# Kernel optimization log

Hardware: AMD Instinct MI355X
Metric: run time of the kernel (lower is better)

The kernel has to match this reference:

```python
import jax, jax.numpy as jnp
import numpy as np

B, T, K = 256, 512, 128


def _reverse_sequence(x, lens, axis_len):
    # Reverse the first lens[b] entries of x[b] along time axis (axis=1); rest unchanged.
    pos = jnp.arange(axis_len)[None, :]              # [1, T]
    idx = jnp.where(pos < lens[:, None], lens[:, None] - 1 - pos, pos)  # [B, T]
    if x.ndim == 3:
        idx = idx[:, :, None]
        idx = jnp.broadcast_to(idx, x.shape)
    return jnp.take_along_axis(x, idx, axis=1)


def setup_inputs() -> dict:
    key = jax.random.key(0)
    k1, k2, k3 = jax.random.split(key, 3)
    potentials = jax.random.normal(k1, (B, T, K), dtype=jnp.float32)
    sequence_lengths = jax.random.randint(k2, (B,), 1, T + 1, dtype=jnp.int32)
    # glorot_uniform for [K, K] transitions
    limit = np.sqrt(6.0 / (K + K))
    transitions = jax.random.uniform(k3, (K, K), dtype=jnp.float32,
                                     minval=-limit, maxval=limit)
    return {"potentials": potentials, "transitions": transitions,
            "sequence_lengths": sequence_lengths}


def _crf_decode(potentials, transitions, sequence_lengths):
    lens = sequence_lengths.astype(jnp.int32)
    num_tags = potentials.shape[-1]
    init_state = potentials[:, 0, :]                 # [B, K]
    inputs = potentials[:, 1:, :]                    # [B, T-1, K]
    lens_m1 = jnp.maximum(0, lens - 1)
    mask = jnp.arange(inputs.shape[1])[None, :] < lens_m1[:, None]  # [B, T-1]

    def fwd_step(state, xm):
        x, m = xm                                    # x [B,K], m [B]
        ts = state[:, :, None] + transitions[None]   # [B, K(prev), K(cur)]
        new_state = x + jnp.max(ts, axis=1)          # [B, K]
        bp = jnp.argmax(ts, axis=1).astype(jnp.int32)
        new_state = jnp.where(m[:, None], new_state, state)
        bp = jnp.where(m[:, None], bp, 0)
        return new_state, bp

    xs = (jnp.swapaxes(inputs, 0, 1), jnp.swapaxes(mask, 0, 1))
    last_score, bps = jax.lax.scan(fwd_step, init_state, xs)
    backpointers = jnp.swapaxes(bps, 0, 1)           # [B, T-1, K]
    backpointers = _reverse_sequence(backpointers, lens_m1, backpointers.shape[1])

    init_tag = jnp.argmax(last_score, axis=1).astype(jnp.int32)  # [B]

    def bwd_step(tag, bp):                           # tag [B], bp [B,K]
        new = jnp.take_along_axis(bp, tag[:, None], axis=1)[:, 0]
        return new, new

    _, tags = jax.lax.scan(bwd_step, init_tag, jnp.swapaxes(backpointers, 0, 1))
    decode_tags = jnp.concatenate([init_tag[:, None], jnp.swapaxes(tags, 0, 1)], axis=1)  # [B,T]
    decode_tags = _reverse_sequence(decode_tags, lens, decode_tags.shape[1])
    best_score = jnp.max(last_score, axis=1)
    return decode_tags, best_score


def reference(potentials, transitions, sequence_lengths):
    decode_tags, _ = _crf_decode(potentials, transitions, sequence_lengths)
    # inference-phase output: one-hot of Viterbi tags
    return jax.nn.one_hot(decode_tags, potentials.shape[-1], dtype=potentials.dtype)
```

## Files before the change

### kernel.cpp

```cpp
#include <hip/hip_runtime.h>

#define B_ 256
#define T_ 512
#define K_ 128
#define NT 256
#define DELTA 0.03125f

template<int CTRL>
__device__ __forceinline__ float dpp_fmax(float v) {
  int iv = __float_as_int(v);
  int t = __builtin_amdgcn_update_dpp(iv, iv, CTRL, 0xF, 0xF, false);
  return fmaxf(v, __int_as_float(t));
}
__device__ __forceinline__ float rlanef(float v, int lane) {
  return __int_as_float(__builtin_amdgcn_readlane(__float_as_int(v), lane));
}
__device__ __forceinline__ int popcand(unsigned long long& m0, unsigned long long& m1) {
  if (m0) { int c = __ffsll(m0) - 1; m0 &= m0 - 1; return c; }
  int c = __ffsll(m1) - 1; m1 &= m1 - 1; return c + 64;
}

__global__ __launch_bounds__(NT) void viterbi_fused(
    const float* __restrict__ pot,
    const float* __restrict__ trans,
    const int*   __restrict__ lens,
    float* __restrict__ out)
{
  extern __shared__ __align__(16) char smem[];
  float2*         Tp   = (float2*)smem;
  unsigned char*  bp   = (unsigned char*)(smem + 65536);
  unsigned short* code = (unsigned short*)(smem + 130944);
  unsigned char*  tags = (unsigned char*)(smem + 131968);
  int*            scr  = (int*)(smem + 132480);

  const int tid = threadIdx.x;
  const int b   = blockIdx.x;
  const int L   = lens[b];
  const float* potb = pot + (size_t)b * T_ * K_;

  float mn = INFINITY, mx = -INFINITY;
  for (int e = tid; e < K_ * 64; e += NT) {
    const int i = e >> 6, ll = e & 63;
    const float a = trans[i * K_ + ll];
    const float c = trans[i * K_ + ll + 64];
    Tp[e] = make_float2(a, c);
    mn = fminf(mn, fminf(a, c));
    mx = fmaxf(mx, fmaxf(a, c));
  }
  float* red = (float*)bp;
  red[tid] = mn; red[NT + tid] = mx;
  __syncthreads();

  if (tid < 64) {
    const int l = tid;
    float rmn = INFINITY, rmx = -INFINITY;
#pragma unroll
    for (int i = 0; i < 4; ++i) {
      rmn = fminf(rmn, red[i * 64 + l]);
      rmx = fmaxf(rmx, red[256 + i * 64 + l]);
    }
    for (int d = 1; d < 64; d <<= 1) {
      rmn = fminf(rmn, __shfl_xor(rmn, d));
      rmx = fmaxf(rmx, __shfl_xor(rmx, d));
    }
    const float Rng = (rmx - rmn) + DELTA;

    float s0 = potb[l], s1 = potb[64 + l];

    float e0_0, e1_0, e0_1, e1_1, e0_2, e1_2, e0_3, e1_3;
    float e0_4, e1_4, e0_5, e1_5, e0_6, e1_6, e0_7, e1_7;
#define PLOAD(KK)                                                     \
    { int idx = 1 + KK; idx = (idx < L) ? idx : (L - 1);              \
      const float* pp = potb + idx * K_;                              \
      e0_##KK = pp[l]; e1_##KK = pp[64 + l]; }
    PLOAD(0) PLOAD(1) PLOAD(2) PLOAD(3) PLOAD(4) PLOAD(5) PLOAD(6) PLOAD(7)

#define VSTEP(KK, PREF)                                                        \
    {                                                                          \
      float lm = fmaxf(s0, s1);                                                \
      lm = dpp_fmax<0x121>(lm);                                                \
      lm = dpp_fmax<0x122>(lm);                                                \
      lm = dpp_fmax<0x124>(lm);                                                \
      lm = dpp_fmax<0x128>(lm);                                                \
      lm = dpp_fmax<0x142>(lm);                                                \
      lm = dpp_fmax<0x143>(lm);                                                \
      const float M = rlanef(lm, 63);                                          \
      const float thr = M - Rng;                                               \
      unsigned long long c0m = __ballot(s0 >= thr);                            \
      unsigned long long c1m = __ballot(s1 >= thr);                            \
      int nc = __popcll(c0m) + __popcll(c1m);                                  \
      if (nc == 0) { c0m = ~0ull; c1m = ~0ull; nc = 128; }                     \
      const int ca = popcand(c0m, c1m);                                        \
      const float sa = (ca < 64) ? rlanef(s0, ca) : rlanef(s1, ca - 64);       \
      const float2 ta = Tp[(ca << 6) + l];                                     \
      if (nc == 1) {                                                           \
        const float a0 = sa + ta.x, a1 = sa + ta.y;                            \
        s0 = e0_##KK + a0; s1 = e1_##KK + a1;                                  \
        if (l == 0) code[t + KK - 1] = (unsigned short)ca;                     \
      } else {                                                                 \
        const int cb = popcand(c0m, c1m);                                      \
        const float sb = (cb < 64) ? rlanef(s0, cb) : rlanef(s1, cb - 64);     \
        const float2 tb = Tp[(cb << 6) + l];                                   \
        int cc = ca, cd = ca; float scv = sa, sdv = sa;                        \
        float2 tc = ta, td = ta;                                               \
        if (nc >= 3) { cc = popcand(c0m, c1m);                                 \
          scv = (cc < 64) ? rlanef(s0, cc) : rlanef(s1, cc - 64);              \
          tc = Tp[(cc << 6) + l]; }                                            \
        if (nc >= 4) { cd = popcand(c0m, c1m);                                 \
          sdv = (cd < 64) ? rlanef(s0, cd) : rlanef(s1, cd - 64);              \
          td = Tp[(cd << 6) + l]; }                                            \
        float m0 = sa + ta.x, m1 = sa + ta.y; int i0 = ca, i1 = ca;            \
        { const float v0 = sb + tb.x, v1 = sb + tb.y;                          \
          if (v0 > m0) { m0 = v0; i0 = cb; }                                   \
          if (v1 > m1) { m1 = v1; i1 = cb; } }                                 \
        if (nc >= 3) { const float v0 = scv + tc.x, v1 = scv + tc.y;           \
          if (v0 > m0) { m0 = v0; i0 = cc; }                                   \
          if (v1 > m1) { m1 = v1; i1 = cc; } }                                 \
        if (nc >= 4) { const float v0 = sdv + td.x, v1 = sdv + td.y;           \
          if (v0 > m0) { m0 = v0; i0 = cd; }                                   \
          if (v1 > m1) { m1 = v1; i1 = cd; } }                                 \
        int rem = nc - 4;                                                      \
        while (rem-- > 0) {                                                    \
          const int c = popcand(c0m, c1m);                                     \
          const float sv = (c < 64) ? rlanef(s0, c) : rlanef(s1, c - 64);      \
          const float2 tv = Tp[(c << 6) + l];                                  \
          const float v0 = sv + tv.x, v1 = sv + tv.y;                          \
          if (v0 > m0) { m0 = v0; i0 = c; }                                    \
          if (v1 > m1) { m1 = v1; i1 = c; }                                    \
        }                                                                      \
        s0 = e0_##KK + m0; s1 = e1_##KK + m1;                                  \
        bp[(t + KK - 1) * K_ + l]      = (unsigned char)i0;                    \
        bp[(t + KK - 1) * K_ + 64 + l] = (unsigned char)i1;                    \
        if (l == 0) code[t + KK - 1] = 0xFFFF;                                 \
      }                                                                        \
      if (PREF) {                                                              \
        int idx = t + KK + 8; idx = (idx < L) ? idx : (L - 1);                 \
        const float* pp = potb + idx * K_;                                     \
        e0_##KK = pp[l]; e1_##KK = pp[64 + l];                                 \
      }                                                                        \
    }

    int t = 1;
    while (t + 8 <= L) {
      VSTEP(0, true) VSTEP(1, true) VSTEP(2, true) VSTEP(3, true)
      VSTEP(4, true) VSTEP(5, true) VSTEP(6, true) VSTEP(7, true)
      t += 8;
    }
    if (t + 0 < L) VSTEP(0, false)
    if (t + 1 < L) VSTEP(1, false)
    if (t + 2 < L) VSTEP(2, false)
    if (t + 3 < L) VSTEP(3, false)
    if (t + 4 < L) VSTEP(4, false)
    if (t + 5 < L) VSTEP(5, false)
    if (t + 6 < L) VSTEP(6, false)

    float bv = s0; int bi = l;
    if (s1 > bv) { bv = s1; bi = l + 64; }
    for (int d = 1; d < 64; d <<= 1) {
      const float ov = __shfl_xor(bv, d);
      const int   oi = __shfl_xor(bi, d);
      if (ov > bv || (ov == bv && oi < bi)) { bv = ov; bi = oi; }
    }
    if (l == 0) { tags[L - 1] = (unsigned char)bi; scr[0] = bi; }
  }
  __syncthreads();

  const int bestTag = scr[0];
  for (int p = L + tid; p < T_; p += NT) tags[p] = 0;
  for (int p = tid; p < L - 1; p += NT) {
    const unsigned short c = code[p];
    if (c != 0xFFFF) {
      int tg = c;
      tags[p] = (unsigned char)tg;
      int q = p - 1;
      while (q >= 0 && code[q] == 0xFFFF) {
        tg = bp[q * K_ + tg];
        tags[q] = (unsigned char)tg;
        --q;
      }
    }
  }
  if (tid == 0 && L >= 2) {
    int tg = bestTag;
    int q = L - 2;
    while (q >= 0 && code[q] == 0xFFFF) {
      tg = bp[q * K_ + tg];
      tags[q] = (unsigned char)tg;
      --q;
    }
  }
  __syncthreads();

  float4* o4 = (float4*)(out + (size_t)b * T_ * K_);
  for (int i = tid; i < T_ * K_ / 4; i += NT) {
    const int p  = i >> 5;
    const int tg = tags[p];
    const int k  = (i & 31) * 4;
    float4 v;
    v.x = (k     == tg) ? 1.0f : 0.0f;
    v.y = (k + 1 == tg) ? 1.0f : 0.0f;
    v.z = (k + 2 == tg) ? 1.0f : 0.0f;
    v.w = (k + 3 == tg) ? 1.0f : 0.0f;
    o4[i] = v;
  }
}

extern "C" void kernel_launch(void* const* d_in, const int* in_sizes, int n_in,
                              void* d_out, int out_size, void* d_ws, size_t ws_size,
                              hipStream_t stream) {
  const float* pot   = (const float*)d_in[0];
  const float* trans = (const float*)d_in[1];
  const int*   lens  = (const int*)d_in[2];
  float* out = (float*)d_out;

  viterbi_fused<<<B_, NT, 132608, stream>>>(pot, trans, lens, out);
}
```

Measured before the change: 311.0 us.

## Use inline-asm loads with vmcnt waits and write padded one-hot rows during forward pass

Replaces the compiler-generated potential prefetch loads with inline-asm global loads followed by explicit s_waitcnt vmcnt(14), so the 8-step-ahead prefetches stay in flight and the compiler cannot insert conservative full waits. The three idle waves now write the one-hot rows for positions past the sequence length (tag 0) while wave 0 runs the Viterbi recursion, and the final output loop covers only the first L rows. This overlaps the padding output stores with the serial forward pass and removes a source of memory stalls. In exchange, correctness now depends on hand-counted vmcnt values matching the exact number of outstanding loads.

```diff
diff --git a/kernel.cpp b/kernel.cpp
--- a/kernel.cpp
+++ b/kernel.cpp
@@ -19,6 +19,9 @@
   if (m0) { int c = __ffsll(m0) - 1; m0 &= m0 - 1; return c; }
   int c = __ffsll(m1) - 1; m1 &= m1 - 1; return c + 64;
 }
+
+#define GLOAD(dst, p) \
+  asm volatile("global_load_dword %0, %1, off" : "=v"(dst) : "v"(p))
 
 __global__ __launch_bounds__(NT) void viterbi_fused(
     const float* __restrict__ pot,
@@ -37,6 +40,7 @@
   const int b   = blockIdx.x;
   const int L   = lens[b];
   const float* potb = pot + (size_t)b * T_ * K_;
+  float4* o4 = (float4*)(out + (size_t)b * T_ * K_);
 
   float mn = INFINITY, mx = -INFINITY;
   for (int e = tid; e < K_ * 64; e += NT) {
@@ -53,6 +57,23 @@
 
   if (tid < 64) {
     const int l = tid;
+
+    float s0, s1;
+    {
+      const float* p0 = potb + l;
+      const float* p1 = potb + 64 + l;
+      GLOAD(s0, p0); GLOAD(s1, p1);
+      asm volatile("s_waitcnt vmcnt(0)" : "+v"(s0), "+v"(s1));
+    }
+
+    float e0_0, e1_0, e0_1, e1_1, e0_2, e1_2, e0_3, e1_3;
+    float e0_4, e1_4, e0_5, e1_5, e0_6, e1_6, e0_7, e1_7;
+#define PLOAD(KK)                                                       \
+    { int idx = 1 + KK; idx = (idx < L) ? idx : (L - 1);                \
+      const float* pp = potb + idx * K_ + l;                            \
+      GLOAD(e0_##KK, pp); GLOAD(e1_##KK, pp + 64); }
+    PLOAD(0) PLOAD(1) PLOAD(2) PLOAD(3) PLOAD(4) PLOAD(5) PLOAD(6) PLOAD(7)
+
     float rmn = INFINITY, rmx = -INFINITY;
 #pragma unroll
     for (int i = 0; i < 4; ++i) {
@@ -65,18 +86,10 @@
     }
     const float Rng = (rmx - rmn) + DELTA;
 
-    float s0 = potb[l], s1 = potb[64 + l];
-
-    float e0_0, e1_0, e0_1, e1_1, e0_2, e1_2, e0_3, e1_3;
-    float e0_4, e1_4, e0_5, e1_5, e0_6, e1_6, e0_7, e1_7;
-#define PLOAD(KK)                                                     \
-    { int idx = 1 + KK; idx = (idx < L) ? idx : (L - 1);              \
-      const float* pp = potb + idx * K_;                              \
-      e0_##KK = pp[l]; e1_##KK = pp[64 + l]; }
-    PLOAD(0) PLOAD(1) PLOAD(2) PLOAD(3) PLOAD(4) PLOAD(5) PLOAD(6) PLOAD(7)
-
-#define VSTEP(KK, PREF)                                                        \
+#define VSTEP(KK, MAIN)                                                        \
     {                                                                          \
+      if (MAIN)                                                                \
+        asm volatile("s_waitcnt vmcnt(14)" : "+v"(e0_##KK), "+v"(e1_##KK));    \
       float lm = fmaxf(s0, s1);                                                \
       lm = dpp_fmax<0x121>(lm);                                                \
       lm = dpp_fmax<0x122>(lm);                                                \
@@ -133,10 +146,10 @@
         bp[(t + KK - 1) * K_ + 64 + l] = (unsigned char)i1;                    \
         if (l == 0) code[t + KK - 1] = 0xFFFF;                                 \
       }                                                                        \
-      if (PREF) {                                                              \
+      if (MAIN) {                                                              \
         int idx = t + KK + 8; idx = (idx < L) ? idx : (L - 1);                 \
-        const float* pp = potb + idx * K_;                                     \
-        e0_##KK = pp[l]; e1_##KK = pp[64 + l];                                 \
+        const float* pp = potb + idx * K_ + l;                                 \
+        GLOAD(e0_##KK, pp); GLOAD(e1_##KK, pp + 64);                           \
       }                                                                        \
     }
 
@@ -146,6 +159,11 @@
       VSTEP(4, true) VSTEP(5, true) VSTEP(6, true) VSTEP(7, true)
       t += 8;
     }
+    asm volatile("s_waitcnt vmcnt(0)"
+      : "+v"(e0_0), "+v"(e1_0), "+v"(e0_1), "+v"(e1_1),
+        "+v"(e0_2), "+v"(e1_2), "+v"(e0_3), "+v"(e1_3),
+        "+v"(e0_4), "+v"(e1_4), "+v"(e0_5), "+v"(e1_5),
+        "+v"(e0_6), "+v"(e1_6), "+v"(e0_7), "+v"(e1_7));
     if (t + 0 < L) VSTEP(0, false)
     if (t + 1 < L) VSTEP(1, false)
     if (t + 2 < L) VSTEP(2, false)
@@ -162,11 +180,19 @@
       if (ov > bv || (ov == bv && oi < bi)) { bv = ov; bi = oi; }
     }
     if (l == 0) { tags[L - 1] = (unsigned char)bi; scr[0] = bi; }
+  } else {
+    const int wtid = tid - 64;
+    const int n4 = (T_ - L) * 32;
+    for (int e = wtid; e < n4; e += 192) {
+      const int row = L + (e >> 5);
+      const int q   = e & 31;
+      float4 v = make_float4(q == 0 ? 1.0f : 0.0f, 0.0f, 0.0f, 0.0f);
+      o4[row * 32 + q] = v;
+    }
   }
   __syncthreads();
 
   const int bestTag = scr[0];
-  for (int p = L + tid; p < T_; p += NT) tags[p] = 0;
   for (int p = tid; p < L - 1; p += NT) {
     const unsigned short c = code[p];
     if (c != 0xFFFF) {
@@ -191,8 +217,7 @@
   }
   __syncthreads();
 
-  float4* o4 = (float4*)(out + (size_t)b * T_ * K_);
-  for (int i = tid; i < T_ * K_ / 4; i += NT) {
+  for (int i = tid; i < (L << 5); i += NT) {
     const int p  = i >> 5;
     const int tg = tags[p];
     const int k  = (i & 31) * 4;
```

New measurement: 307.8 us. Within noise of the previous version (-1.0%).
